# Optimization experiments

Measured on AMD Instinct MI355X. Metric: run time of the kernel, lower is better.

## Reference

```python
import jax, jax.numpy as jnp
import numpy as np

TOP_K = 4  # num_experts_per_tok


def setup_inputs() -> dict:
    key = jax.random.key(0)
    ks = jax.random.split(key, 7)
    B, S, H, E, I = 1, 1024, 1024, 16, 2880
    scale_h = 1.0 / np.sqrt(H)
    scale_i = 1.0 / np.sqrt(I)
    return {
        "hidden_states": jax.random.normal(ks[0], (B, S, H), jnp.float32),
        "gate_w": jax.random.normal(ks[1], (E, H), jnp.float32) * scale_h,
        "gate_b": jax.random.normal(ks[2], (E,), jnp.float32) * 0.01,
        "gate_up_proj": jax.random.normal(ks[3], (E, H, 2 * I), jnp.float32) * scale_h,
        "gate_up_proj_bias": jax.random.normal(ks[4], (E, 2 * I), jnp.float32) * 0.01,
        "down_proj": jax.random.normal(ks[5], (E, I, H), jnp.float32) * scale_i,
        "down_proj_bias": jax.random.normal(ks[6], (E, H), jnp.float32) * 0.01,
    }


def reference(hidden_states, gate_w, gate_b, gate_up_proj, gate_up_proj_bias,
              down_proj, down_proj_bias):
    B, S, H = hidden_states.shape
    E = gate_w.shape[0]
    I = down_proj.shape[1]
    x = hidden_states.reshape(-1, H)  # [T, H]
    T = x.shape[0]

    # Router: top-k logits, softmax over selected logits only
    router_logits = x @ gate_w.T + gate_b          # [T, E]
    top_vals, top_idx = jax.lax.top_k(router_logits, TOP_K)
    routing_weights = jax.nn.softmax(top_vals, axis=-1)  # [T, K]

    # Combine matrix: C[t, e] = routing weight of expert e for token t (0 if unselected)
    C = jnp.zeros((T, E), x.dtype).at[jnp.arange(T)[:, None], top_idx].add(routing_weights)

    # Dense per-expert MLP (reference computes all experts, combine masks unselected)
    gu = jnp.einsum('th,ehf->tef', x, gate_up_proj) + gate_up_proj_bias[None]  # [T, E, 2I]
    gate, up = gu[..., :I], gu[..., I:]
    inter = jax.nn.silu(gate) * up                                            # [T, E, I]
    expert_out = jnp.einsum('tei,eih->teh', inter, down_proj) + down_proj_bias[None]  # [T, E, H]
    out = jnp.einsum('teh,te->th', expert_out, C)                             # [T, H]

    return out.reshape(B, S, H), router_logits
```

## Files before the change

kernel.cpp:

```cpp
#include <hip/hip_runtime.h>
#include <hip/hip_bf16.h>
#include <stdint.h>

#define T_TOK 1024
#define HDIM  1024
#define NEXP  16
#define IDIM  2880
#define GU_COLS (2*IDIM)
#define TOPK  4

using short4v  = __attribute__((ext_vector_type(4))) short;
using short8   = __attribute__((ext_vector_type(8))) short;
using ushort4v = __attribute__((ext_vector_type(4))) unsigned short;
using f32x4    = __attribute__((ext_vector_type(4))) float;

__device__ __forceinline__ unsigned short f2b(float f) {
    union { float f; unsigned u; } x; x.f = f;
    unsigned r = x.u + 0x7FFFu + ((x.u >> 16) & 1u);
    return (unsigned short)(r >> 16);
}

typedef const __attribute__((address_space(1))) unsigned int* gas1_t;
typedef __attribute__((address_space(3))) unsigned int* las3_t;
__device__ __forceinline__ void gload16(const void* g, void* l) {
    __builtin_amdgcn_global_load_lds((gas1_t)g, (las3_t)l, 16, 0, 0);
}

__global__ __launch_bounds__(256) void router_kernel(
    const float* __restrict__ x, const float* __restrict__ gw,
    const float* __restrict__ gb, float* __restrict__ logits_out,
    int* __restrict__ counts, int* __restrict__ lists, float* __restrict__ wts,
    unsigned short* __restrict__ xb, float* __restrict__ out)
{
    int t = blockIdx.x;
    int tid = threadIdx.x;
    const float* xr = x + (size_t)t * HDIM;
    {
        float4 v = *(const float4*)(xr + tid * 4);
        ushort4v b; b.x = f2b(v.x); b.y = f2b(v.y); b.z = f2b(v.z); b.w = f2b(v.w);
        *(ushort4v*)(xb + (size_t)t * HDIM + tid * 4) = b;
        float4 z = make_float4(0.f, 0.f, 0.f, 0.f);
        *(float4*)(out + (size_t)t * HDIM + tid * 4) = z;
    }
    int e = tid >> 4;
    int l16 = tid & 15;
    const float* wr = gw + (size_t)e * HDIM;
    float p = 0.f;
    for (int h = l16; h < HDIM; h += 16) p += xr[h] * wr[h];
    p += __shfl_xor(p, 8);
    p += __shfl_xor(p, 4);
    p += __shfl_xor(p, 2);
    p += __shfl_xor(p, 1);
    __shared__ float sl[NEXP];
    if (l16 == 0) {
        float v = p + gb[e];
        sl[e] = v;
        logits_out[t * NEXP + e] = v;
    }
    __syncthreads();
    if (tid == 0) {
        float v[NEXP];
#pragma unroll
        for (int i = 0; i < NEXP; ++i) v[i] = sl[i];
        int idx[TOPK]; float tv[TOPK];
        unsigned used = 0;
#pragma unroll
        for (int k = 0; k < TOPK; ++k) {
            float best = -__builtin_inff(); int bi = 0;
#pragma unroll
            for (int i = 0; i < NEXP; ++i)
                if (!((used >> i) & 1u) && v[i] > best) { best = v[i]; bi = i; }
            used |= 1u << bi; idx[k] = bi; tv[k] = best;
        }
        float m = tv[0];
        float ex[TOPK], s = 0.f;
#pragma unroll
        for (int k = 0; k < TOPK; ++k) { ex[k] = expf(tv[k] - m); s += ex[k]; }
#pragma unroll
        for (int k = 0; k < TOPK; ++k) {
            float w = ex[k] / s;
            int slot = atomicAdd(&counts[idx[k]], 1);
            lists[idx[k] * T_TOK + slot] = t;
            wts[idx[k] * T_TOK + slot] = w;
        }
    }
}

__global__ void offsets_kernel(const int* __restrict__ counts, int* __restrict__ offsets)
{
    if (threadIdx.x == 0) {
        int o = 0;
        for (int e = 0; e < NEXP; ++e) { offsets[e] = o; o += counts[e]; }
        offsets[NEXP] = o;
    }
}

__global__ __launch_bounds__(512) void gu_kernel(
    const unsigned short* __restrict__ xb, const float* __restrict__ gup,
    const float* __restrict__ gub, const int* __restrict__ counts,
    const int* __restrict__ offsets, const int* __restrict__ lists,
    unsigned short* __restrict__ inter)
{
    int bid = blockIdx.x;
    int nt = bid % 90;
    int t2 = bid / 90;
    int e  = t2 & 15;
    int mt = t2 >> 4;
    int ne = counts[e];
    if (mt * 256 >= ne) return;

    int tid = threadIdx.x;
    int wave = tid >> 6, lane = tid & 63;
    int l16 = lane & 15, lq = lane >> 4;

    __shared__ int tokid[256];
    __shared__ unsigned short As[256 * 64];
    __shared__ unsigned short Bs[64 * 64];

    if (tid < 256) {
        int slot = mt * 256 + tid;
        tokid[tid] = (slot < ne) ? lists[e * T_TOK + slot] : lists[e * T_TOK];
    }
    __syncthreads();

    const float* gup_e = gup + (size_t)e * HDIM * GU_COLS;

    int at = tid - 256;
    const unsigned short* asrc[8];
    if (tid >= 256) {
#pragma unroll
        for (int i = 0; i < 8; ++i) {
            int s = at + i * 256;
            int row = s >> 3, c = s & 7;
            asrc[i] = xb + (size_t)tokid[row] * HDIM + ((c ^ (row & 7)) * 8);
        }
    }
    int nb = tid & 15, kb = tid >> 4;
    const float* bsrc = nullptr;
    if (tid < 256) {
        int n0 = nb * 4;
        size_t col = (n0 < 32) ? (size_t)(nt * 32 + n0) : (size_t)(IDIM + nt * 32 + (n0 - 32));
        bsrc = gup_e + (size_t)(kb * 4) * GU_COLS + col;
    }

    f32x4 acc[2][4];
#pragma unroll
    for (int i = 0; i < 2; ++i)
#pragma unroll
        for (int f = 0; f < 4; ++f) acc[i][f] = (f32x4){0.f, 0.f, 0.f, 0.f};

    for (int kk = 0; kk < HDIM; kk += 64) {
        __syncthreads();
        if (tid >= 256) {
#pragma unroll
            for (int i = 0; i < 8; ++i)
                gload16(asrc[i] + kk, As + ((size_t)(at + i * 256)) * 8);
        } else {
            const float* sp = bsrc + (size_t)kk * GU_COLS;
            float4 r0 = *(const float4*)(sp);
            float4 r1 = *(const float4*)(sp + GU_COLS);
            float4 r2 = *(const float4*)(sp + 2 * GU_COLS);
            float4 r3 = *(const float4*)(sp + 3 * GU_COLS);
#pragma unroll
            for (int j = 0; j < 4; ++j) {
                int n = nb * 4 + j;
                int slot = kb ^ (n & 15);
                float e0 = (&r0.x)[j], e1 = (&r1.x)[j], e2 = (&r2.x)[j], e3 = (&r3.x)[j];
                ushort4v b; b.x = f2b(e0); b.y = f2b(e1); b.z = f2b(e2); b.w = f2b(e3);
                *(ushort4v*)&Bs[n * 64 + slot * 4] = b;
            }
        }
        __syncthreads();
#pragma unroll
        for (int ks = 0; ks < 2; ++ks) {
            short8 a[2], b[4];
#pragma unroll
            for (int i = 0; i < 2; ++i) {
                int row = wave * 32 + i * 16 + l16;
                int q = ks * 4 + lq;
                a[i] = *(const short8*)&As[row * 64 + ((q ^ (row & 7)) * 8)];
            }
#pragma unroll
            for (int f = 0; f < 4; ++f) {
                int n = f * 16 + l16;
                int u0 = (ks * 8 + lq * 2) ^ (n & 15);
                int u1 = (ks * 8 + lq * 2 + 1) ^ (n & 15);
                short4v h0 = *(const short4v*)&Bs[n * 64 + u0 * 4];
                short4v h1 = *(const short4v*)&Bs[n * 64 + u1 * 4];
                b[f] = __builtin_shufflevector(h0, h1, 0, 1, 2, 3, 4, 5, 6, 7);
            }
#pragma unroll
            for (int i = 0; i < 2; ++i)
#pragma unroll
                for (int f = 0; f < 4; ++f)
                    acc[i][f] = __builtin_amdgcn_mfma_f32_16x16x32_bf16(a[i], b[f], acc[i][f], 0, 0, 0);
        }
    }

    int off = offsets[e];
    const float* gbe = gub + (size_t)e * GU_COLS;
#pragma unroll
    for (int j = 0; j < 2; ++j) {
        int col = j * 16 + l16;
        float bg = gbe[nt * 32 + col];
        float bu = gbe[IDIM + nt * 32 + col];
#pragma unroll
        for (int i = 0; i < 2; ++i)
#pragma unroll
            for (int r = 0; r < 4; ++r) {
                int row = wave * 32 + i * 16 + lq * 4 + r;
                int slot = mt * 256 + row;
                if (slot < ne) {
                    float g = acc[i][j][r] + bg;
                    float u = acc[i][j + 2][r] + bu;
                    float sg = g / (1.f + expf(-g));
                    inter[(size_t)(off + slot) * IDIM + nt * 32 + col] = f2b(sg * u);
                }
            }
    }
}

__global__ __launch_bounds__(512) void down_kernel(
    const unsigned short* __restrict__ inter, const float* __restrict__ dw,
    const float* __restrict__ db, const int* __restrict__ counts,
    const int* __restrict__ offsets, const int* __restrict__ lists,
    const float* __restrict__ wts, float* __restrict__ out)
{
    int bid = blockIdx.x;
    int ht = bid & 15;
    int t2 = bid >> 4;
    int e  = t2 & 15;
    int mt = t2 >> 4;
    int ne = counts[e];
    if (mt * 256 >= ne) return;

    int tid = threadIdx.x;
    int wave = tid >> 6, lane = tid & 63;
    int l16 = lane & 15, lq = lane >> 4;

    __shared__ int tokid[256];
    __shared__ float twt[256];
    __shared__ unsigned short As[256 * 64];
    __shared__ unsigned short Bs[64 * 64];

    int off = offsets[e];
    if (tid < 256) {
        int slot = mt * 256 + tid;
        tokid[tid] = (slot < ne) ? lists[e * T_TOK + slot] : -1;
        twt[tid]   = (slot < ne) ? wts[e * T_TOK + slot] : 0.f;
    }
    __syncthreads();

    const float* dw_e = dw + (size_t)e * IDIM * HDIM;

    int at = tid - 256;
    const unsigned short* asrc[8];
    if (tid >= 256) {
#pragma unroll
        for (int i = 0; i < 8; ++i) {
            int s = at + i * 256;
            int row = s >> 3, c = s & 7;
            int slotr = mt * 256 + row; if (slotr >= ne) slotr = ne - 1;
            asrc[i] = inter + (size_t)(off + slotr) * IDIM + ((c ^ (row & 7)) * 8);
        }
    }
    int nb = tid & 15, kb = tid >> 4;
    const float* bsrc = nullptr;
    if (tid < 256)
        bsrc = dw_e + (size_t)(kb * 4) * HDIM + ht * 64 + nb * 4;

    f32x4 acc[2][4];
#pragma unroll
    for (int i = 0; i < 2; ++i)
#pragma unroll
        for (int f = 0; f < 4; ++f) acc[i][f] = (f32x4){0.f, 0.f, 0.f, 0.f};

    for (int kk = 0; kk < IDIM; kk += 64) {
        __syncthreads();
        if (tid >= 256) {
#pragma unroll
            for (int i = 0; i < 8; ++i)
                gload16(asrc[i] + kk, As + ((size_t)(at + i * 256)) * 8);
        } else {
            const float* sp = bsrc + (size_t)kk * HDIM;
            float4 r0 = *(const float4*)(sp);
            float4 r1 = *(const float4*)(sp + HDIM);
            float4 r2 = *(const float4*)(sp + 2 * HDIM);
            float4 r3 = *(const float4*)(sp + 3 * HDIM);
#pragma unroll
            for (int j = 0; j < 4; ++j) {
                int n = nb * 4 + j;
                int slot = kb ^ (n & 15);
                float e0 = (&r0.x)[j], e1 = (&r1.x)[j], e2 = (&r2.x)[j], e3 = (&r3.x)[j];
                ushort4v b; b.x = f2b(e0); b.y = f2b(e1); b.z = f2b(e2); b.w = f2b(e3);
                *(ushort4v*)&Bs[n * 64 + slot * 4] = b;
            }
        }
        __syncthreads();
#pragma unroll
        for (int ks = 0; ks < 2; ++ks) {
            short8 a[2], b[4];
#pragma unroll
            for (int i = 0; i < 2; ++i) {
                int row = wave * 32 + i * 16 + l16;
                int q = ks * 4 + lq;
                a[i] = *(const short8*)&As[row * 64 + ((q ^ (row & 7)) * 8)];
            }
#pragma unroll
            for (int f = 0; f < 4; ++f) {
                int n = f * 16 + l16;
                int u0 = (ks * 8 + lq * 2) ^ (n & 15);
                int u1 = (ks * 8 + lq * 2 + 1) ^ (n & 15);
                short4v h0 = *(const short4v*)&Bs[n * 64 + u0 * 4];
                short4v h1 = *(const short4v*)&Bs[n * 64 + u1 * 4];
                b[f] = __builtin_shufflevector(h0, h1, 0, 1, 2, 3, 4, 5, 6, 7);
            }
#pragma unroll
            for (int i = 0; i < 2; ++i)
#pragma unroll
                for (int f = 0; f < 4; ++f)
                    acc[i][f] = __builtin_amdgcn_mfma_f32_16x16x32_bf16(a[i], b[f], acc[i][f], 0, 0, 0);
        }
    }

    const float* db_e = db + (size_t)e * HDIM;
#pragma unroll
    for (int f = 0; f < 4; ++f) {
        int h = ht * 64 + f * 16 + l16;
        float bias = db_e[h];
#pragma unroll
        for (int i = 0; i < 2; ++i)
#pragma unroll
            for (int r = 0; r < 4; ++r) {
                int row = wave * 32 + i * 16 + lq * 4 + r;
                int tk = tokid[row];
                if (tk >= 0)
                    atomicAdd(out + (size_t)tk * HDIM + h, twt[row] * (acc[i][f][r] + bias));
            }
    }
}

extern "C" void kernel_launch(void* const* d_in, const int* in_sizes, int n_in,
                              void* d_out, int out_size, void* d_ws, size_t ws_size,
                              hipStream_t stream)
{
    const float* x   = (const float*)d_in[0];
    const float* gw  = (const float*)d_in[1];
    const float* gb  = (const float*)d_in[2];
    const float* gup = (const float*)d_in[3];
    const float* gub = (const float*)d_in[4];
    const float* dw  = (const float*)d_in[5];
    const float* db  = (const float*)d_in[6];

    float* out        = (float*)d_out;
    float* logits_out = out + (size_t)T_TOK * HDIM;

    char* ws = (char*)d_ws;
    int*   counts  = (int*)(ws + 0);
    int*   offsets = (int*)(ws + 256);
    int*   lists   = (int*)(ws + 512);
    float* wts     = (float*)(ws + 512 + 65536);
    unsigned short* xb    = (unsigned short*)(ws + 131584);
    unsigned short* inter = (unsigned short*)(ws + 2228736);

    hipMemsetAsync(counts, 0, 64, stream);

    router_kernel<<<T_TOK, 256, 0, stream>>>(x, gw, gb, logits_out, counts, lists, wts, xb, out);
    offsets_kernel<<<1, 64, 0, stream>>>(counts, offsets);
    gu_kernel<<<4 * NEXP * 90, 512, 0, stream>>>(xb, gup, gub, counts, offsets, lists, inter);
    down_kernel<<<4 * NEXP * 16, 512, 0, stream>>>(inter, dw, db, counts, offsets, lists, wts, out);
}
```

Baseline: 329.6 us.

## Software-pipeline fp32 weight loads into registers with split waitcnt barriers

```diff
diff --git a/kernel.cpp b/kernel.cpp
--- a/kernel.cpp
+++ b/kernel.cpp
@@ -25,6 +25,19 @@
 __device__ __forceinline__ void gload16(const void* g, void* l) {
     __builtin_amdgcn_global_load_lds((gas1_t)g, (las3_t)l, 16, 0, 0);
 }
+
+#define BAR_PRESTAGE() do { \
+    asm volatile("s_waitcnt lgkmcnt(0)" ::: "memory"); \
+    __builtin_amdgcn_s_barrier(); \
+    __builtin_amdgcn_sched_barrier(0); \
+} while (0)
+
+#define BAR_PRECOMPUTE(is_a_wave) do { \
+    if (is_a_wave) asm volatile("s_waitcnt vmcnt(0)" ::: "memory"); \
+    else           asm volatile("s_waitcnt lgkmcnt(0)" ::: "memory"); \
+    __builtin_amdgcn_s_barrier(); \
+    __builtin_amdgcn_sched_barrier(0); \
+} while (0)
 
 __global__ __launch_bounds__(256) void router_kernel(
     const float* __restrict__ x, const float* __restrict__ gw,
@@ -112,6 +125,7 @@
     int tid = threadIdx.x;
     int wave = tid >> 6, lane = tid & 63;
     int l16 = lane & 15, lq = lane >> 4;
+    bool is_a_wave = (tid >= 256);
 
     __shared__ int tokid[256];
     __shared__ unsigned short As[256 * 64];
@@ -127,7 +141,7 @@
 
     int at = tid - 256;
     const unsigned short* asrc[8];
-    if (tid >= 256) {
+    if (is_a_wave) {
 #pragma unroll
         for (int i = 0; i < 8; ++i) {
             int s = at + i * 256;
@@ -137,7 +151,7 @@
     }
     int nb = tid & 15, kb = tid >> 4;
     const float* bsrc = nullptr;
-    if (tid < 256) {
+    if (!is_a_wave) {
         int n0 = nb * 4;
         size_t col = (n0 < 32) ? (size_t)(nt * 32 + n0) : (size_t)(IDIM + nt * 32 + (n0 - 32));
         bsrc = gup_e + (size_t)(kb * 4) * GU_COLS + col;
@@ -149,28 +163,54 @@
 #pragma unroll
         for (int f = 0; f < 4; ++f) acc[i][f] = (f32x4){0.f, 0.f, 0.f, 0.f};
 
+    float4  brf0, brf1, brf2, brf3;
+    ushort4v bc0, bc1, bc2, bc3;
+
+    if (!is_a_wave) {
+        brf0 = *(const float4*)(bsrc);
+        brf1 = *(const float4*)(bsrc + GU_COLS);
+        brf2 = *(const float4*)(bsrc + 2 * GU_COLS);
+        brf3 = *(const float4*)(bsrc + 3 * GU_COLS);
+        bc0 = (ushort4v){f2b(brf0.x), f2b(brf1.x), f2b(brf2.x), f2b(brf3.x)};
+        bc1 = (ushort4v){f2b(brf0.y), f2b(brf1.y), f2b(brf2.y), f2b(brf3.y)};
+        bc2 = (ushort4v){f2b(brf0.z), f2b(brf1.z), f2b(brf2.z), f2b(brf3.z)};
+        bc3 = (ushort4v){f2b(brf0.w), f2b(brf1.w), f2b(brf2.w), f2b(brf3.w)};
+        const float* sp = bsrc + (size_t)64 * GU_COLS;
+        brf0 = *(const float4*)(sp);
+        brf1 = *(const float4*)(sp + GU_COLS);
+        brf2 = *(const float4*)(sp + 2 * GU_COLS);
+        brf3 = *(const float4*)(sp + 3 * GU_COLS);
+    }
+
     for (int kk = 0; kk < HDIM; kk += 64) {
-        __syncthreads();
-        if (tid >= 256) {
+        BAR_PRESTAGE();
+        if (is_a_wave) {
 #pragma unroll
             for (int i = 0; i < 8; ++i)
                 gload16(asrc[i] + kk, As + ((size_t)(at + i * 256)) * 8);
         } else {
-            const float* sp = bsrc + (size_t)kk * GU_COLS;
-            float4 r0 = *(const float4*)(sp);
-            float4 r1 = *(const float4*)(sp + GU_COLS);
-            float4 r2 = *(const float4*)(sp + 2 * GU_COLS);
-            float4 r3 = *(const float4*)(sp + 3 * GU_COLS);
-#pragma unroll
-            for (int j = 0; j < 4; ++j) {
-                int n = nb * 4 + j;
-                int slot = kb ^ (n & 15);
-                float e0 = (&r0.x)[j], e1 = (&r1.x)[j], e2 = (&r2.x)[j], e3 = (&r3.x)[j];
-                ushort4v b; b.x = f2b(e0); b.y = f2b(e1); b.z = f2b(e2); b.w = f2b(e3);
-                *(ushort4v*)&Bs[n * 64 + slot * 4] = b;
-            }
-        }
-        __syncthreads();
+            *(ushort4v*)&Bs[(nb * 4 + 0) * 64 + (kb ^ ((nb * 4 + 0) & 15)) * 4] = bc0;
+            *(ushort4v*)&Bs[(nb * 4 + 1) * 64 + (kb ^ ((nb * 4 + 1) & 15)) * 4] = bc1;
+            *(ushort4v*)&Bs[(nb * 4 + 2) * 64 + (kb ^ ((nb * 4 + 2) & 15)) * 4] = bc2;
+            *(ushort4v*)&Bs[(nb * 4 + 3) * 64 + (kb ^ ((nb * 4 + 3) & 15)) * 4] = bc3;
+        }
+        BAR_PRECOMPUTE(is_a_wave);
+        if (!is_a_wave) {
+            if (kk + 64 < HDIM) {
+                bc0 = (ushort4v){f2b(brf0.x), f2b(brf1.x), f2b(brf2.x), f2b(brf3.x)};
+                bc1 = (ushort4v){f2b(brf0.y), f2b(brf1.y), f2b(brf2.y), f2b(brf3.y)};
+                bc2 = (ushort4v){f2b(brf0.z), f2b(brf1.z), f2b(brf2.z), f2b(brf3.z)};
+                bc3 = (ushort4v){f2b(brf0.w), f2b(brf1.w), f2b(brf2.w), f2b(brf3.w)};
+            }
+            if (kk + 128 < HDIM) {
+                const float* sp = bsrc + (size_t)(kk + 128) * GU_COLS;
+                brf0 = *(const float4*)(sp);
+                brf1 = *(const float4*)(sp + GU_COLS);
+                brf2 = *(const float4*)(sp + 2 * GU_COLS);
+                brf3 = *(const float4*)(sp + 3 * GU_COLS);
+            }
+        }
+        __builtin_amdgcn_s_setprio(1);
 #pragma unroll
         for (int ks = 0; ks < 2; ++ks) {
             short8 a[2], b[4];
@@ -195,6 +235,7 @@
                 for (int f = 0; f < 4; ++f)
                     acc[i][f] = __builtin_amdgcn_mfma_f32_16x16x32_bf16(a[i], b[f], acc[i][f], 0, 0, 0);
         }
+        __builtin_amdgcn_s_setprio(0);
     }
 
     int off = offsets[e];
@@ -227,16 +268,16 @@
     const float* __restrict__ wts, float* __restrict__ out)
 {
     int bid = blockIdx.x;
-    int ht = bid & 15;
-    int t2 = bid >> 4;
-    int e  = t2 & 15;
-    int mt = t2 >> 4;
+    int ht  = bid & 15;
+    int e   = (bid >> 4) & 15;
+    int mt  = bid >> 8;
     int ne = counts[e];
     if (mt * 256 >= ne) return;
 
     int tid = threadIdx.x;
     int wave = tid >> 6, lane = tid & 63;
     int l16 = lane & 15, lq = lane >> 4;
+    bool is_a_wave = (tid >= 256);
 
     __shared__ int tokid[256];
     __shared__ float twt[256];
@@ -255,7 +296,7 @@
 
     int at = tid - 256;
     const unsigned short* asrc[8];
-    if (tid >= 256) {
+    if (is_a_wave) {
 #pragma unroll
         for (int i = 0; i < 8; ++i) {
             int s = at + i * 256;
@@ -266,7 +307,7 @@
     }
     int nb = tid & 15, kb = tid >> 4;
     const float* bsrc = nullptr;
-    if (tid < 256)
+    if (!is_a_wave)
         bsrc = dw_e + (size_t)(kb * 4) * HDIM + ht * 64 + nb * 4;
 
     f32x4 acc[2][4];
@@ -275,28 +316,54 @@
 #pragma unroll
         for (int f = 0; f < 4; ++f) acc[i][f] = (f32x4){0.f, 0.f, 0.f, 0.f};
 
+    float4  brf0, brf1, brf2, brf3;
+    ushort4v bc0, bc1, bc2, bc3;
+
+    if (!is_a_wave) {
+        brf0 = *(const float4*)(bsrc);
+        brf1 = *(const float4*)(bsrc + HDIM);
+        brf2 = *(const float4*)(bsrc + 2 * HDIM);
+        brf3 = *(const float4*)(bsrc + 3 * HDIM);
+        bc0 = (ushort4v){f2b(brf0.x), f2b(brf1.x), f2b(brf2.x), f2b(brf3.x)};
+        bc1 = (ushort4v){f2b(brf0.y), f2b(brf1.y), f2b(brf2.y), f2b(brf3.y)};
+        bc2 = (ushort4v){f2b(brf0.z), f2b(brf1.z), f2b(brf2.z), f2b(brf3.z)};
+        bc3 = (ushort4v){f2b(brf0.w), f2b(brf1.w), f2b(brf2.w), f2b(brf3.w)};
+        const float* sp = bsrc + (size_t)64 * HDIM;
+        brf0 = *(const float4*)(sp);
+        brf1 = *(const float4*)(sp + HDIM);
+        brf2 = *(const float4*)(sp + 2 * HDIM);
+        brf3 = *(const float4*)(sp + 3 * HDIM);
+    }
+
     for (int kk = 0; kk < IDIM; kk += 64) {
-        __syncthreads();
-        if (tid >= 256) {
+        BAR_PRESTAGE();
+        if (is_a_wave) {
 #pragma unroll
             for (int i = 0; i < 8; ++i)
                 gload16(asrc[i] + kk, As + ((size_t)(at + i * 256)) * 8);
         } else {
-            const float* sp = bsrc + (size_t)kk * HDIM;
-            float4 r0 = *(const float4*)(sp);
-            float4 r1 = *(const float4*)(sp + HDIM);
-            float4 r2 = *(const float4*)(sp + 2 * HDIM);
-            float4 r3 = *(const float4*)(sp + 3 * HDIM);
-#pragma unroll
-            for (int j = 0; j < 4; ++j) {
-                int n = nb * 4 + j;
-                int slot = kb ^ (n & 15);
-                float e0 = (&r0.x)[j], e1 = (&r1.x)[j], e2 = (&r2.x)[j], e3 = (&r3.x)[j];
-                ushort4v b; b.x = f2b(e0); b.y = f2b(e1); b.z = f2b(e2); b.w = f2b(e3);
-                *(ushort4v*)&Bs[n * 64 + slot * 4] = b;
-            }
-        }
-        __syncthreads();
+            *(ushort4v*)&Bs[(nb * 4 + 0) * 64 + (kb ^ ((nb * 4 + 0) & 15)) * 4] = bc0;
+            *(ushort4v*)&Bs[(nb * 4 + 1) * 64 + (kb ^ ((nb * 4 + 1) & 15)) * 4] = bc1;
+            *(ushort4v*)&Bs[(nb * 4 + 2) * 64 + (kb ^ ((nb * 4 + 2) & 15)) * 4] = bc2;
+            *(ushort4v*)&Bs[(nb * 4 + 3) * 64 + (kb ^ ((nb * 4 + 3) & 15)) * 4] = bc3;
+        }
+        BAR_PRECOMPUTE(is_a_wave);
+        if (!is_a_wave) {
+            if (kk + 64 < IDIM) {
+                bc0 = (ushort4v){f2b(brf0.x), f2b(brf1.x), f2b(brf2.x), f2b(brf3.x)};
+                bc1 = (ushort4v){f2b(brf0.y), f2b(brf1.y), f2b(brf2.y), f2b(brf3.y)};
+                bc2 = (ushort4v){f2b(brf0.z), f2b(brf1.z), f2b(brf2.z), f2b(brf3.z)};
+                bc3 = (ushort4v){f2b(brf0.w), f2b(brf1.w), f2b(brf2.w), f2b(brf3.w)};
+            }
+            if (kk + 128 < IDIM) {
+                const float* sp = bsrc + (size_t)(kk + 128) * HDIM;
+                brf0 = *(const float4*)(sp);
+                brf1 = *(const float4*)(sp + HDIM);
+                brf2 = *(const float4*)(sp + 2 * HDIM);
+                brf3 = *(const float4*)(sp + 3 * HDIM);
+            }
+        }
+        __builtin_amdgcn_s_setprio(1);
 #pragma unroll
         for (int ks = 0; ks < 2; ++ks) {
             short8 a[2], b[4];
@@ -321,6 +388,7 @@
                 for (int f = 0; f < 4; ++f)
                     acc[i][f] = __builtin_amdgcn_mfma_f32_16x16x32_bf16(a[i], b[f], acc[i][f], 0, 0, 0);
         }
+        __builtin_amdgcn_s_setprio(0);
     }
 
     const float* db_e = db + (size_t)e * HDIM;
```

Result: no change. 325.4 us (-1.3%).
